# Kernel optimization log

Hardware: AMD Instinct MI355X
Metric: run time of the kernel (lower is better)

## Reference

```python
import jax, jax.numpy as jnp
import numpy as np

D_MODEL = 1024
NUM_HEADS = 16
D_K = D_MODEL // NUM_HEADS
B, S = 2, 2048


def setup_inputs() -> dict:
    key = jax.random.key(0)
    ks = jax.random.split(key, 12)
    s = 1.0 / np.sqrt(D_MODEL)
    inp = {
        "Q": jax.random.normal(ks[0], (B, S, D_MODEL), jnp.float32),
        "K": jax.random.normal(ks[1], (B, S, D_MODEL), jnp.float32),
        "V": jax.random.normal(ks[2], (B, S, D_MODEL), jnp.float32),
        "mask": jnp.tril(jnp.ones((S, S), jnp.int32))[None, None],  # causal [1,1,S,S]
        "W_Q": jax.random.uniform(ks[3], (D_MODEL, D_MODEL), jnp.float32, -s, s),
        "b_Q": jax.random.uniform(ks[4], (D_MODEL,), jnp.float32, -s, s),
        "W_K": jax.random.uniform(ks[5], (D_MODEL, D_MODEL), jnp.float32, -s, s),
        "b_K": jax.random.uniform(ks[6], (D_MODEL,), jnp.float32, -s, s),
        "W_V": jax.random.uniform(ks[7], (D_MODEL, D_MODEL), jnp.float32, -s, s),
        "b_V": jax.random.uniform(ks[8], (D_MODEL,), jnp.float32, -s, s),
        "W_O": jax.random.uniform(ks[9], (D_MODEL, D_MODEL), jnp.float32, -s, s),
        "b_O": jax.random.uniform(ks[10], (D_MODEL,), jnp.float32, -s, s),
    }
    return inp


def _split_heads(x):
    b, s, _ = x.shape
    return x.reshape(b, s, NUM_HEADS, D_K).transpose(0, 2, 1, 3)  # [B,H,S,d_k]


def reference(Q, K, V, mask, W_Q, b_Q, W_K, b_K, W_V, b_V, W_O, b_O):
    q = _split_heads(Q @ W_Q.T + b_Q)
    k = _split_heads(K @ W_K.T + b_K)
    v = _split_heads(V @ W_V.T + b_V)
    scores = jnp.einsum("bhqd,bhkd->bhqk", q, k) / jnp.sqrt(jnp.float32(D_K))
    scores = jnp.where(mask == 0, -jnp.inf, scores)
    attn = jax.nn.softmax(scores, axis=-1)
    out = jnp.einsum("bhqk,bhkd->bhqd", attn, v)
    out = out.transpose(0, 2, 1, 3).reshape(Q.shape[0], Q.shape[1], D_MODEL)
    out = out @ W_O.T + b_O
    return out, attn
```

## Files before the change

kernel.cpp:

```cpp
#include <hip/hip_runtime.h>

typedef __attribute__((ext_vector_type(4))) float f32x4;
typedef __attribute__((ext_vector_type(8))) __bf16 bf16x8;
typedef __attribute__((ext_vector_type(4))) __bf16 bf16x4;

#define D_MODEL 1024
#define S_LEN 2048
#define MROWS 4096

#if __has_builtin(__builtin_amdgcn_exp2f)
#define EXP2F(x) __builtin_amdgcn_exp2f(x)
#else
#define EXP2F(x) exp2f(x)
#endif

#define QSCALE 0.1803368801111204f

__device__ __forceinline__ void gload_lds16(const void* g, void* l) {
  __builtin_amdgcn_global_load_lds(
      (const __attribute__((address_space(1))) unsigned int*)g,
      (__attribute__((address_space(3))) unsigned int*)l, 16, 0, 0);
}

__global__ void cvt_qkv(const float* __restrict__ Q, const float* __restrict__ K,
                        const float* __restrict__ V, __bf16* __restrict__ dst) {
  const int y = blockIdx.y;
  const float* src = (y == 0) ? Q : (y == 1) ? K : V;
  __bf16* d = dst + (size_t)y * (MROWS * D_MODEL);
  const int n4 = MROWS * D_MODEL / 4;
  for (int i = blockIdx.x * blockDim.x + threadIdx.x; i < n4; i += 512 * 256) {
    f32x4 v = *(const f32x4*)(src + i * 4);
    bf16x4 o;
#pragma unroll
    for (int j = 0; j < 4; ++j) o[j] = (__bf16)v[j];
    *(bf16x4*)(d + i * 4) = o;
  }
}

__global__ void cvt_w(const float* __restrict__ w0, const float* __restrict__ w1,
                      const float* __restrict__ w2, const float* __restrict__ w3,
                      __bf16* __restrict__ dst) {
  const int y = blockIdx.y;
  const float* src = (y == 0) ? w0 : (y == 1) ? w1 : (y == 2) ? w2 : w3;
  const float sc = (y == 0) ? QSCALE : 1.0f;
  __bf16* d = dst + (size_t)y * (D_MODEL * D_MODEL);
  const int n4 = D_MODEL * D_MODEL / 4;
  for (int i = blockIdx.x * blockDim.x + threadIdx.x; i < n4; i += 256 * 256) {
    f32x4 v = *(const f32x4*)(src + i * 4);
    bf16x4 o;
#pragma unroll
    for (int j = 0; j < 4; ++j) o[j] = (__bf16)(v[j] * sc);
    *(bf16x4*)(d + i * 4) = o;
  }
}

__device__ __forceinline__ void gemm_core64(const __bf16* __restrict__ A,
                                            const __bf16* __restrict__ B,
                                            __bf16* As, __bf16* Bs,
                                            int m0, int n0, f32x4 (&acc)[4][4]) {
  const int tid = threadIdx.x;
  const int lane = tid & 63, wid = tid >> 6;
  const int li = lane & 15, g = lane >> 4;
  const int wr = wid >> 1, wc = wid & 1;
  const int srow = tid >> 3, sc = tid & 7;
  const int scol = (sc ^ (srow & 7)) * 8;
  const int sw = li & 7;
  for (int k0 = 0; k0 < D_MODEL; k0 += 64) {
#pragma unroll
    for (int i = 0; i < 4; ++i) {
      const int r = i * 32 + srow;
      gload_lds16(A + (size_t)(m0 + r) * D_MODEL + k0 + scol, (char*)As + i * 4096 + wid * 1024);
      gload_lds16(B + (size_t)(n0 + r) * D_MODEL + k0 + scol, (char*)Bs + i * 4096 + wid * 1024);
    }
    __syncthreads();
#pragma unroll
    for (int kk = 0; kk < 2; ++kk) {
      bf16x8 af[4], bfr[4];
#pragma unroll
      for (int i = 0; i < 4; ++i) {
        af[i]  = *(const bf16x8*)&As[(wr * 64 + i * 16 + li) * 64 + (((kk * 4 + g) ^ sw) * 8)];
        bfr[i] = *(const bf16x8*)&Bs[(wc * 64 + i * 16 + li) * 64 + (((kk * 4 + g) ^ sw) * 8)];
      }
      __builtin_amdgcn_s_setprio(1);
#pragma unroll
      for (int i = 0; i < 4; ++i)
#pragma unroll
        for (int j = 0; j < 4; ++j)
          acc[i][j] = __builtin_amdgcn_mfma_f32_16x16x32_bf16(af[i], bfr[j], acc[i][j], 0, 0, 0);
      __builtin_amdgcn_s_setprio(0);
    }
    __syncthreads();
  }
}

__global__ __launch_bounds__(256) void qkv_gemm(
    const __bf16* __restrict__ Qb, const __bf16* __restrict__ Kb, const __bf16* __restrict__ Vb,
    const __bf16* __restrict__ Wq, const __bf16* __restrict__ Wk, const __bf16* __restrict__ Wv,
    const float* __restrict__ bq, const float* __restrict__ bk, const float* __restrict__ bv,
    __bf16* __restrict__ qp, __bf16* __restrict__ kp, __bf16* __restrict__ vt) {
  __shared__ __bf16 As[128 * 64];
  __shared__ __bf16 Bs[128 * 64];
  const int z = blockIdx.z;
  const __bf16* A = (z == 0) ? Qb : (z == 1) ? Kb : Vb;
  const __bf16* B = (z == 0) ? Wq : (z == 1) ? Wk : Wv;
  const float* bias = (z == 0) ? bq : (z == 1) ? bk : bv;
  const float bsc = (z == 0) ? QSCALE : 1.0f;
  const int m0 = blockIdx.x * 128, n0 = blockIdx.y * 128;
  f32x4 acc[4][4] = {};
  gemm_core64(A, B, As, Bs, m0, n0, acc);

  const int lane = threadIdx.x & 63, wid = threadIdx.x >> 6;
  const int li = lane & 15, g = lane >> 4;
  const int wr = wid >> 1, wc = wid & 1;
#pragma unroll
  for (int j = 0; j < 4; ++j) {
    const int n = n0 + wc * 64 + j * 16 + li;
    const float bv_ = bias[n] * bsc;
#pragma unroll
    for (int i = 0; i < 4; ++i) {
#pragma unroll
      for (int r = 0; r < 4; ++r) {
        const int m = m0 + wr * 64 + i * 16 + g * 4 + r;
        const float v = acc[i][j][r] + bv_;
        if (z == 2) {
          const int bb = m >> 11, s = m & 2047;
          vt[((size_t)(bb * D_MODEL + n)) * S_LEN + s] = (__bf16)v;
        } else {
          __bf16* o = (z == 0) ? qp : kp;
          o[(size_t)m * D_MODEL + n] = (__bf16)v;
        }
      }
    }
  }
}

__global__ __launch_bounds__(256) void o_gemm(const __bf16* __restrict__ ctx,
                                              const __bf16* __restrict__ Wo,
                                              const float* __restrict__ bo,
                                              float* __restrict__ out) {
  __shared__ __bf16 As[128 * 64];
  __shared__ __bf16 Bs[128 * 64];
  const int m0 = blockIdx.x * 128, n0 = blockIdx.y * 128;
  f32x4 acc[4][4] = {};
  gemm_core64(ctx, Wo, As, Bs, m0, n0, acc);

  const int lane = threadIdx.x & 63, wid = threadIdx.x >> 6;
  const int li = lane & 15, g = lane >> 4;
  const int wr = wid >> 1, wc = wid & 1;
#pragma unroll
  for (int j = 0; j < 4; ++j) {
    const int n = n0 + wc * 64 + j * 16 + li;
    const float bv_ = bo[n];
#pragma unroll
    for (int i = 0; i < 4; ++i)
#pragma unroll
      for (int r = 0; r < 4; ++r) {
        const int m = m0 + wr * 64 + i * 16 + g * 4 + r;
        out[(size_t)m * D_MODEL + n] = acc[i][j][r] + bv_;
      }
  }
}

__global__ __launch_bounds__(256) void attn_fused5(const __bf16* __restrict__ qp,
                                                   const __bf16* __restrict__ kp,
                                                   const __bf16* __restrict__ vt,
                                                   float* __restrict__ attn,
                                                   __bf16* __restrict__ ctx) {
  const int bid = blockIdx.x;
  const int qt = 31 - (bid >> 5);
  const int bh = bid & 31;
  const int b = bh >> 4, h = bh & 15;
  const int tid = threadIdx.x, lane = tid & 63, wid = tid >> 6;
  const int li = lane & 15, g = lane >> 4;
  const int sw = li & 7;
  const int qrow0 = qt * 64 + wid * 16;
  const float NEG_INF = -__builtin_inff();

  __shared__ __bf16 kv_lds[4][64 * 64];
  __shared__ __bf16 p_lds[4][16 * 64];

  const __bf16* qbase = qp + ((size_t)(b * S_LEN + qrow0 + li)) * D_MODEL + h * 64 + g * 8;
  const bf16x8 qf0 = *(const bf16x8*)qbase;
  const bf16x8 qf1 = *(const bf16x8*)(qbase + 32);

  const int srow = tid >> 3;
  const int sc = tid & 7;
  const int schunk = (sc ^ (srow & 7)) * 8;
  const __bf16* kpb = kp + (size_t)(b * S_LEN) * D_MODEL + h * 64 + schunk;
  const __bf16* vpb = vt + (size_t)(bh * 64) * S_LEN + schunk;

  auto stage_k = [&](int kt, int bufi) {
#pragma unroll
    for (int i = 0; i < 2; ++i)
      gload_lds16(kpb + (size_t)(kt * 64 + i * 32 + srow) * D_MODEL,
                  (char*)kv_lds[bufi] + i * 4096 + wid * 1024);
  };
  auto stage_v = [&](int kt, int bufi) {
#pragma unroll
    for (int i = 0; i < 2; ++i)
      gload_lds16(vpb + (size_t)(i * 32 + srow) * S_LEN + kt * 64,
                  (char*)kv_lds[2 + bufi] + i * 4096 + wid * 1024);
  };
  auto qk_tile = [&](const __bf16* kb, f32x4 (&sv)[4]) {
    __builtin_amdgcn_s_setprio(1);
#pragma unroll
    for (int sub = 0; sub < 4; ++sub) {
      const __bf16* rp = kb + (sub * 16 + li) * 64;
      const bf16x8 k0 = *(const bf16x8*)(rp + ((g ^ sw) * 8));
      const bf16x8 k1 = *(const bf16x8*)(rp + (((4 + g) ^ sw) * 8));
      f32x4 t = {};
      t = __builtin_amdgcn_mfma_f32_16x16x32_bf16(qf0, k0, t, 0, 0, 0);
      t = __builtin_amdgcn_mfma_f32_16x16x32_bf16(qf1, k1, t, 0, 0, 0);
      sv[sub] = t;
    }
    __builtin_amdgcn_s_setprio(0);
  };
  const int rowl = wid * 16 + g * 4;
  auto mask_diag = [&](f32x4 (&sv)[4]) {
#pragma unroll
    for (int sub = 0; sub < 4; ++sub) {
      const int coll = sub * 16 + li;
#pragma unroll
      for (int r = 0; r < 4; ++r)
        if (coll > rowl + r) sv[sub][r] = NEG_INF;
    }
  };

  const int nt = qt + 1;

  float esum[4] = {0.f, 0.f, 0.f, 0.f};
  stage_k(0, 0);
  if (nt > 1) stage_k(1, 1);
  for (int p0 = 0; p0 < nt; p0 += 2) {
    const int cs = (p0 >> 1) & 1;
    __syncthreads();
    const int ns = cs ^ 1;
    if (p0 + 2 < nt) stage_k(p0 + 2, ns * 2);
    if (p0 + 3 < nt) stage_k(p0 + 3, ns * 2 + 1);
    {
      f32x4 sv[4];
      qk_tile(kv_lds[cs * 2], sv);
      if (p0 == qt) mask_diag(sv);
#pragma unroll
      for (int r = 0; r < 4; ++r)
        esum[r] += (EXP2F(sv[0][r]) + EXP2F(sv[1][r])) + (EXP2F(sv[2][r]) + EXP2F(sv[3][r]));
    }
    if (p0 + 1 < nt) {
      f32x4 sv[4];
      qk_tile(kv_lds[cs * 2 + 1], sv);
      if (p0 + 1 == qt) mask_diag(sv);
#pragma unroll
      for (int r = 0; r < 4; ++r)
        esum[r] += (EXP2F(sv[0][r]) + EXP2F(sv[1][r])) + (EXP2F(sv[2][r]) + EXP2F(sv[3][r]));
    }
  }
  float inv_l[4];
#pragma unroll
  for (int r = 0; r < 4; ++r) {
    float e = esum[r];
    e += __shfl_xor(e, 1);
    e += __shfl_xor(e, 2);
    e += __shfl_xor(e, 4);
    e += __shfl_xor(e, 8);
    inv_l[r] = 1.f / e;
  }

  float* attn_bh = attn + (size_t)bh * S_LEN * S_LEN;
  float* arp[4];
#pragma unroll
  for (int r = 0; r < 4; ++r)
    arp[r] = attn_bh + (size_t)(qrow0 + g * 4 + r) * S_LEN + li;

  __bf16* pw = &p_lds[wid][0];
  f32x4 acc[4] = {};

  __syncthreads();
  int buf = 0;
  stage_k(0, 0);
  stage_v(0, 0);
  for (int kt = 0; kt < nt; ++kt) {
    __syncthreads();
    stage_k(kt + 1, buf ^ 1);
    stage_v(kt + 1, buf ^ 1);
    f32x4 sv[4];
    qk_tile(kv_lds[buf], sv);
    if (kt == qt) mask_diag(sv);
    const int colbase = kt * 64;
#pragma unroll
    for (int r = 0; r < 4; ++r) {
      const int prow = g * 4 + r;
#pragma unroll
      for (int sub = 0; sub < 4; ++sub) {
        const float p = EXP2F(sv[sub][r]) * inv_l[r];
        arp[r][colbase + sub * 16] = p;
        pw[prow * 64 + (((sub * 2 + (li >> 3)) ^ (prow & 7)) * 8) + (li & 7)] = (__bf16)p;
      }
    }
    __builtin_amdgcn_s_setprio(1);
    const bf16x8 pa0 = *(const bf16x8*)&pw[li * 64 + ((g ^ sw) * 8)];
    const bf16x8 pa1 = *(const bf16x8*)&pw[li * 64 + (((4 + g) ^ sw) * 8)];
    const __bf16* vb = kv_lds[2 + buf];
#pragma unroll
    for (int c4 = 0; c4 < 4; ++c4) {
      const __bf16* vrp = vb + (c4 * 16 + li) * 64;
      const bf16x8 vf0 = *(const bf16x8*)(vrp + ((g ^ sw) * 8));
      const bf16x8 vf1 = *(const bf16x8*)(vrp + (((4 + g) ^ sw) * 8));
      acc[c4] = __builtin_amdgcn_mfma_f32_16x16x32_bf16(pa0, vf0, acc[c4], 0, 0, 0);
      acc[c4] = __builtin_amdgcn_mfma_f32_16x16x32_bf16(pa1, vf1, acc[c4], 0, 0, 0);
    }
    __builtin_amdgcn_s_setprio(0);
    buf ^= 1;
  }

#pragma unroll
  for (int c4 = 0; c4 < 4; ++c4)
#pragma unroll
    for (int r = 0; r < 4; ++r)
      ctx[((size_t)(b * S_LEN) + qrow0 + g * 4 + r) * D_MODEL + h * 64 + c4 * 16 + li] =
          (__bf16)acc[c4][r];

  const int c0 = nt * 64;
  for (int r = 0; r < 16; ++r) {
    float* rowp = attn_bh + (size_t)(qrow0 + r) * S_LEN;
    for (int col = c0 + lane * 4; col < S_LEN; col += 256) {
      f32x4 z = {};
      *(f32x4*)(rowp + col) = z;
    }
  }
}

extern "C" void kernel_launch(void* const* d_in, const int* in_sizes, int n_in,
                              void* d_out, int out_size, void* d_ws, size_t ws_size,
                              hipStream_t stream) {
  const float* Q  = (const float*)d_in[0];
  const float* K  = (const float*)d_in[1];
  const float* V  = (const float*)d_in[2];
  const float* W_Q = (const float*)d_in[4];
  const float* b_Q = (const float*)d_in[5];
  const float* W_K = (const float*)d_in[6];
  const float* b_K = (const float*)d_in[7];
  const float* W_V = (const float*)d_in[8];
  const float* b_V = (const float*)d_in[9];
  const float* W_O = (const float*)d_in[10];
  const float* b_O = (const float*)d_in[11];

  char* ws = (char*)d_ws;
  __bf16* Qb  = (__bf16*)(ws + 0);
  __bf16* Wq  = (__bf16*)(ws + 25165824);
  __bf16* qp  = (__bf16*)(ws + 33554432);
  __bf16* kp  = (__bf16*)(ws + 41943040);
  __bf16* vtb = (__bf16*)(ws + 50331648);
  __bf16* ctx = (__bf16*)(ws + 58720256);
  __bf16* Kb = Qb + (size_t)MROWS * D_MODEL;
  __bf16* Vb = Kb + (size_t)MROWS * D_MODEL;
  __bf16* Wk = Wq + (size_t)D_MODEL * D_MODEL;
  __bf16* Wv = Wk + (size_t)D_MODEL * D_MODEL;
  __bf16* Wo = Wv + (size_t)D_MODEL * D_MODEL;

  float* out = (float*)d_out;
  float* attn = out + (size_t)MROWS * D_MODEL;

  cvt_qkv<<<dim3(512, 3), 256, 0, stream>>>(Q, K, V, Qb);
  cvt_w<<<dim3(256, 4), 256, 0, stream>>>(W_Q, W_K, W_V, W_O, Wq);

  qkv_gemm<<<dim3(32, 8, 3), 256, 0, stream>>>(Qb, Kb, Vb, Wq, Wk, Wv,
                                               b_Q, b_K, b_V, qp, kp, vtb);

  attn_fused5<<<1024, 256, 0, stream>>>(qp, kp, vtb, attn, ctx);

  o_gemm<<<dim3(32, 8), 256, 0, stream>>>(ctx, Wo, b_O, out);
}
```

Baseline: 253.6 us.

## Split first-pass softmax denominator across waves by key tile instead of query band

The first pass that computes softmax row sums now has each wave handle a different key tile for all four query bands, instead of every wave walking all key tiles for its own 16 rows. Row sums are then combined across waves through shared memory. The goal is to cut the redundant LDS reads of K in the first pass, since each K fragment now feeds four MFMAs. The cost is more Q registers, single-buffered staging with two barriers per round, and clamped redundant loads when the tile count is not a multiple of four.

```diff
diff --git a/kernel.cpp b/kernel.cpp
--- a/kernel.cpp
+++ b/kernel.cpp
@@ -161,11 +161,11 @@
   }
 }
 
-__global__ __launch_bounds__(256) void attn_fused5(const __bf16* __restrict__ qp,
-                                                   const __bf16* __restrict__ kp,
-                                                   const __bf16* __restrict__ vt,
-                                                   float* __restrict__ attn,
-                                                   __bf16* __restrict__ ctx) {
+__global__ __launch_bounds__(256) void attn_fused10(const __bf16* __restrict__ qp,
+                                                    const __bf16* __restrict__ kp,
+                                                    const __bf16* __restrict__ vt,
+                                                    float* __restrict__ attn,
+                                                    __bf16* __restrict__ ctx) {
   const int bid = blockIdx.x;
   const int qt = 31 - (bid >> 5);
   const int bh = bid & 31;
@@ -176,12 +176,10 @@
   const int qrow0 = qt * 64 + wid * 16;
   const float NEG_INF = -__builtin_inff();
 
-  __shared__ __bf16 kv_lds[4][64 * 64];
-  __shared__ __bf16 p_lds[4][16 * 64];
-
-  const __bf16* qbase = qp + ((size_t)(b * S_LEN + qrow0 + li)) * D_MODEL + h * 64 + g * 8;
-  const bf16x8 qf0 = *(const bf16x8*)qbase;
-  const bf16x8 qf1 = *(const bf16x8*)(qbase + 32);
+  __shared__ char smem[40960];
+  __bf16 (*kv4)[64 * 64] = (__bf16(*)[64 * 64])smem;
+  float* l_comb = (float*)(smem + 32768);
+  __bf16* p_base = (__bf16*)(smem + 32768);
 
   const int srow = tid >> 3;
   const int sc = tid & 7;
@@ -189,17 +187,101 @@
   const __bf16* kpb = kp + (size_t)(b * S_LEN) * D_MODEL + h * 64 + schunk;
   const __bf16* vpb = vt + (size_t)(bh * 64) * S_LEN + schunk;
 
+  const int nt = qt + 1;
+
+  bf16x8 q0[4], q1[4];
+#pragma unroll
+  for (int band = 0; band < 4; ++band) {
+    const __bf16* qb =
+        qp + ((size_t)(b * S_LEN + qt * 64 + band * 16 + li)) * D_MODEL + h * 64 + g * 8;
+    q0[band] = *(const bf16x8*)qb;
+    q1[band] = *(const bf16x8*)(qb + 32);
+  }
+
+  f32x4 esum[4] = {};
+
+  const int rounds = (nt + 3) >> 2;
+  for (int j = 0; j < rounds; ++j) {
+#pragma unroll
+    for (int i = 0; i < 4; ++i) {
+      int kt_i = 4 * j + i;
+      const int ktc = (kt_i < nt) ? kt_i : (nt - 1);
+#pragma unroll
+      for (int half = 0; half < 2; ++half)
+        gload_lds16(kpb + (size_t)(ktc * 64 + half * 32 + srow) * D_MODEL,
+                    (char*)kv4[i] + half * 4096 + wid * 1024);
+    }
+    __syncthreads();
+    const int kt = 4 * j + wid;
+    if (kt < nt) {
+      const __bf16* kb = kv4[wid];
+#pragma unroll
+      for (int sub = 0; sub < 4; ++sub) {
+        const __bf16* rp = kb + (sub * 16 + li) * 64;
+        const bf16x8 k0 = *(const bf16x8*)(rp + ((g ^ sw) * 8));
+        const bf16x8 k1 = *(const bf16x8*)(rp + (((4 + g) ^ sw) * 8));
+        const int coll = sub * 16 + li;
+#pragma unroll
+        for (int band = 0; band < 4; ++band) {
+          f32x4 t = {};
+          t = __builtin_amdgcn_mfma_f32_16x16x32_bf16(q0[band], k0, t, 0, 0, 0);
+          t = __builtin_amdgcn_mfma_f32_16x16x32_bf16(q1[band], k1, t, 0, 0, 0);
+          if (kt == qt) {
+            const int rowl = band * 16 + g * 4;
+#pragma unroll
+            for (int r = 0; r < 4; ++r)
+              if (coll > rowl + r) t[r] = NEG_INF;
+          }
+#pragma unroll
+          for (int r = 0; r < 4; ++r) esum[band][r] += EXP2F(t[r]);
+        }
+      }
+    }
+    __syncthreads();
+  }
+
+#pragma unroll
+  for (int band = 0; band < 4; ++band)
+#pragma unroll
+    for (int r = 0; r < 4; ++r) {
+      float e = esum[band][r];
+      e += __shfl_xor(e, 1);
+      e += __shfl_xor(e, 2);
+      e += __shfl_xor(e, 4);
+      e += __shfl_xor(e, 8);
+      esum[band][r] = e;
+    }
+  if (li == 0) {
+#pragma unroll
+    for (int band = 0; band < 4; ++band)
+#pragma unroll
+      for (int r = 0; r < 4; ++r)
+        l_comb[wid * 64 + band * 16 + g * 4 + r] = esum[band][r];
+  }
+  __syncthreads();
+  float inv_l[4];
+#pragma unroll
+  for (int r = 0; r < 4; ++r) {
+    const int row = wid * 16 + g * 4 + r;
+    inv_l[r] = 1.f / (l_comb[row] + l_comb[64 + row] + l_comb[128 + row] + l_comb[192 + row]);
+  }
+  __syncthreads();
+
+  const __bf16* qbase = qp + ((size_t)(b * S_LEN + qrow0 + li)) * D_MODEL + h * 64 + g * 8;
+  const bf16x8 qf0 = *(const bf16x8*)qbase;
+  const bf16x8 qf1 = *(const bf16x8*)(qbase + 32);
+
   auto stage_k = [&](int kt, int bufi) {
 #pragma unroll
     for (int i = 0; i < 2; ++i)
       gload_lds16(kpb + (size_t)(kt * 64 + i * 32 + srow) * D_MODEL,
-                  (char*)kv_lds[bufi] + i * 4096 + wid * 1024);
+                  (char*)kv4[bufi] + i * 4096 + wid * 1024);
   };
   auto stage_v = [&](int kt, int bufi) {
 #pragma unroll
     for (int i = 0; i < 2; ++i)
       gload_lds16(vpb + (size_t)(i * 32 + srow) * S_LEN + kt * 64,
-                  (char*)kv_lds[2 + bufi] + i * 4096 + wid * 1024);
+                  (char*)kv4[2 + bufi] + i * 4096 + wid * 1024);
   };
   auto qk_tile = [&](const __bf16* kb, f32x4 (&sv)[4]) {
     __builtin_amdgcn_s_setprio(1);
@@ -215,55 +297,6 @@
     }
     __builtin_amdgcn_s_setprio(0);
   };
-  const int rowl = wid * 16 + g * 4;
-  auto mask_diag = [&](f32x4 (&sv)[4]) {
-#pragma unroll
-    for (int sub = 0; sub < 4; ++sub) {
-      const int coll = sub * 16 + li;
-#pragma unroll
-      for (int r = 0; r < 4; ++r)
-        if (coll > rowl + r) sv[sub][r] = NEG_INF;
-    }
-  };
-
-  const int nt = qt + 1;
-
-  float esum[4] = {0.f, 0.f, 0.f, 0.f};
-  stage_k(0, 0);
-  if (nt > 1) stage_k(1, 1);
-  for (int p0 = 0; p0 < nt; p0 += 2) {
-    const int cs = (p0 >> 1) & 1;
-    __syncthreads();
-    const int ns = cs ^ 1;
-    if (p0 + 2 < nt) stage_k(p0 + 2, ns * 2);
-    if (p0 + 3 < nt) stage_k(p0 + 3, ns * 2 + 1);
-    {
-      f32x4 sv[4];
-      qk_tile(kv_lds[cs * 2], sv);
-      if (p0 == qt) mask_diag(sv);
-#pragma unroll
-      for (int r = 0; r < 4; ++r)
-        esum[r] += (EXP2F(sv[0][r]) + EXP2F(sv[1][r])) + (EXP2F(sv[2][r]) + EXP2F(sv[3][r]));
-    }
-    if (p0 + 1 < nt) {
-      f32x4 sv[4];
-      qk_tile(kv_lds[cs * 2 + 1], sv);
-      if (p0 + 1 == qt) mask_diag(sv);
-#pragma unroll
-      for (int r = 0; r < 4; ++r)
-        esum[r] += (EXP2F(sv[0][r]) + EXP2F(sv[1][r])) + (EXP2F(sv[2][r]) + EXP2F(sv[3][r]));
-    }
-  }
-  float inv_l[4];
-#pragma unroll
-  for (int r = 0; r < 4; ++r) {
-    float e = esum[r];
-    e += __shfl_xor(e, 1);
-    e += __shfl_xor(e, 2);
-    e += __shfl_xor(e, 4);
-    e += __shfl_xor(e, 8);
-    inv_l[r] = 1.f / e;
-  }
 
   float* attn_bh = attn + (size_t)bh * S_LEN * S_LEN;
   float* arp[4];
@@ -271,10 +304,9 @@
   for (int r = 0; r < 4; ++r)
     arp[r] = attn_bh + (size_t)(qrow0 + g * 4 + r) * S_LEN + li;
 
-  __bf16* pw = &p_lds[wid][0];
+  __bf16* pw = p_base + wid * (16 * 64);
   f32x4 acc[4] = {};
 
-  __syncthreads();
   int buf = 0;
   stage_k(0, 0);
   stage_v(0, 0);
@@ -283,8 +315,17 @@
     stage_k(kt + 1, buf ^ 1);
     stage_v(kt + 1, buf ^ 1);
     f32x4 sv[4];
-    qk_tile(kv_lds[buf], sv);
-    if (kt == qt) mask_diag(sv);
+    qk_tile(kv4[buf], sv);
+    if (kt == qt) {
+      const int rowl = wid * 16 + g * 4;
+#pragma unroll
+      for (int sub = 0; sub < 4; ++sub) {
+        const int coll = sub * 16 + li;
+#pragma unroll
+        for (int r = 0; r < 4; ++r)
+          if (coll > rowl + r) sv[sub][r] = NEG_INF;
+      }
+    }
     const int colbase = kt * 64;
 #pragma unroll
     for (int r = 0; r < 4; ++r) {
@@ -299,7 +340,7 @@
     __builtin_amdgcn_s_setprio(1);
     const bf16x8 pa0 = *(const bf16x8*)&pw[li * 64 + ((g ^ sw) * 8)];
     const bf16x8 pa1 = *(const bf16x8*)&pw[li * 64 + (((4 + g) ^ sw) * 8)];
-    const __bf16* vb = kv_lds[2 + buf];
+    const __bf16* vb = kv4[2 + buf];
 #pragma unroll
     for (int c4 = 0; c4 < 4; ++c4) {
       const __bf16* vrp = vb + (c4 * 16 + li) * 64;
@@ -366,7 +407,7 @@
   qkv_gemm<<<dim3(32, 8, 3), 256, 0, stream>>>(Qb, Kb, Vb, Wq, Wk, Wv,
                                                b_Q, b_K, b_V, qp, kp, vtb);
 
-  attn_fused5<<<1024, 256, 0, stream>>>(qp, kp, vtb, attn, ctx);
+  attn_fused10<<<1024, 256, 0, stream>>>(qp, kp, vtb, attn, ctx);
 
   o_gemm<<<dim3(32, 8), 256, 0, stream>>>(ctx, Wo, b_O, out);
 }
```

Result: no change. 254.3 us (+0.3%).
